# Performance work log

Measured on AMD Instinct MI355X. Metric: run time of the kernel, lower is better.

## Reference

```python
import jax, jax.numpy as jnp
import numpy as np

G = 4
N = G * G  # 16 nodes

def _edges():
    e = []
    for i in range(G):
        for j in range(G):
            n = i * G + j
            if j + 1 < G:
                e += [[n, n + 1], [n + 1, n]]
            if i + 1 < G:
                e += [[n, n + G], [n + G, n]]
    # PyG GATConv default add_self_loops=True
    e += [[k, k] for k in range(N)]
    a = np.asarray(e, dtype=np.int32)
    return jnp.asarray(a[:, 0]), jnp.asarray(a[:, 1])

SRC, DST = _edges()  # [E]=64 each


def gat_layer(h, W, att_src, att_dst, bias, concat):
    # h: [B, N, Fin]; W: [Fin, H*C]; att_*: [H, C]
    B = h.shape[0]
    H, C = att_src.shape
    x = (h @ W).reshape(B, N, H, C)
    a_s = (x * att_src).sum(-1)  # [B, N, H]
    a_d = (x * att_dst).sum(-1)
    alpha = jax.nn.leaky_relu(a_s[:, SRC] + a_d[:, DST], negative_slope=0.2)  # [B, E, H]
    alpha = jnp.swapaxes(alpha, 0, 1)  # [E, B, H] (segment ops act on axis 0)
    m = jax.ops.segment_max(alpha, DST, num_segments=N)  # [N, B, H]
    ex = jnp.exp(alpha - m[DST])
    s = jax.ops.segment_sum(ex, DST, num_segments=N)
    w = ex / s[DST]  # softmax over incoming edges per dst node
    msg = w[..., None] * jnp.swapaxes(x, 0, 1)[SRC]  # [E, B, H, C]
    agg = jax.ops.segment_sum(msg, DST, num_segments=N)  # [N, B, H, C]
    agg = jnp.swapaxes(agg, 0, 1)  # [B, N, H, C]
    if concat:
        return agg.reshape(B, N, H * C) + bias
    return agg.mean(axis=2) + bias


def layer_norm(x, g, b, eps=1e-5):
    mu = x.mean(-1, keepdims=True)
    var = ((x - mu) ** 2).mean(-1, keepdims=True)
    return (x - mu) * jax.lax.rsqrt(var + eps) * g + b


def setup_inputs() -> dict:
    key = jax.random.key(0)
    ks = iter(jax.random.split(key, 32))
    B, Cin, Hd, Hh, Dout = 8192, 16, 64, 4, 256
    def gl(k, shape, fan_in):
        return jax.random.normal(k, shape, jnp.float32) * (1.0 / np.sqrt(fan_in))
    inp = {
        'x': jax.random.normal(next(ks), (B, Cin, G, G), jnp.float32),
        'w_in': gl(next(ks), (Cin, Hd), Cin),
        'b_in': jnp.zeros((Hd,), jnp.float32),
        # GAT layer 0: 64 -> 4x64 concat
        'w0': gl(next(ks), (Hd, Hh * Hd), Hd),
        'as0': gl(next(ks), (Hh, Hd), Hd), 'ad0': gl(next(ks), (Hh, Hd), Hd),
        'bias0': jnp.zeros((Hh * Hd,), jnp.float32),
        # GAT layer 1: 256 -> 4x64 concat
        'w1': gl(next(ks), (Hh * Hd, Hh * Hd), Hh * Hd),
        'as1': gl(next(ks), (Hh, Hd), Hd), 'ad1': gl(next(ks), (Hh, Hd), Hd),
        'bias1': jnp.zeros((Hh * Hd,), jnp.float32),
        # GAT layer 2: 256 -> 64 (mean over heads)
        'w2': gl(next(ks), (Hh * Hd, Hh * Hd), Hh * Hd),
        'as2': gl(next(ks), (Hh, Hd), Hd), 'ad2': gl(next(ks), (Hh, Hd), Hd),
        'bias2': jnp.zeros((Hd,), jnp.float32),
        # output MLP: 64 -> 128 -> 256, LN+ReLU after each layer
        'mw1': gl(next(ks), (Hd, Dout // 2), Hd), 'mb1': jnp.zeros((Dout // 2,), jnp.float32),
        'g1': jnp.ones((Dout // 2,), jnp.float32), 'be1': jnp.zeros((Dout // 2,), jnp.float32),
        'mw2': gl(next(ks), (Dout // 2, Dout), Dout // 2), 'mb2': jnp.zeros((Dout,), jnp.float32),
        'g2': jnp.ones((Dout,), jnp.float32), 'be2': jnp.zeros((Dout,), jnp.float32),
    }
    return inp


def reference(x, w_in, b_in, w0, as0, ad0, bias0, w1, as1, ad1, bias1,
              w2, as2, ad2, bias2, mw1, mb1, g1, be1, mw2, mb2, g2, be2):
    B = x.shape[0]
    # grid -> node features: (B,C,H,W) -> (B,H,W,C) -> (B,N,C)
    h = jnp.transpose(x, (0, 2, 3, 1)).reshape(B, N, -1)
    h = jax.nn.relu(h @ w_in + b_in)
    h = gat_layer(h, w0, as0, ad0, bias0, concat=True)
    h = jax.nn.relu(h)  # dropout inactive in eval
    h = gat_layer(h, w1, as1, ad1, bias1, concat=True)
    h = jax.nn.relu(h)
    h = gat_layer(h, w2, as2, ad2, bias2, concat=False)  # [B, N, 64]
    gr = h.mean(axis=1)  # global mean pool over the 16 nodes
    y = jax.nn.relu(layer_norm(gr @ mw1 + mb1, g1, be1))
    y = jax.nn.relu(layer_norm(y @ mw2 + mb2, g2, be2))
    return y
```

## Files before the change

### kernel.cpp

```cpp
#include <hip/hip_runtime.h>

typedef unsigned short u16;
typedef unsigned int   u32;
typedef __attribute__((ext_vector_type(8))) short bf16x8;
typedef __attribute__((ext_vector_type(4))) float f32x4;

#define GPB 4

__constant__ int ADJ_DEG[16] = {3,4,4,3, 4,5,5,4, 4,5,5,4, 3,4,4,3};
__constant__ int ADJ_SRC[16][5] = {
  {0,1,4,0,0},   {1,0,2,5,0},   {2,1,3,6,0},   {3,2,7,0,0},
  {4,5,0,8,0},   {5,4,6,1,9},   {6,5,7,2,10},  {7,6,3,11,0},
  {8,9,4,12,0},  {9,8,10,5,13}, {10,9,11,6,14},{11,10,7,15,0},
  {12,13,8,0,0}, {13,12,14,9,0},{14,13,15,10,0},{15,14,11,0,0}
};

struct SMem {
  char hA[64*512];
  char hBT[4*256*32];
  union {
    struct { float h0f[64][17]; float w_in_s[16][64]; } pre;
    struct { float asd[64][4][2]; char ptb[8192]; } post;
    struct { float grs[4][64]; float z1[4][128]; float red[2][8][2]; } mlp;
  } u;
};

__device__ __forceinline__ int swz(int row, int b) { return (row << 9) + (b ^ ((row & 7) << 4)); }
__device__ __forceinline__ u32 f2bf1(float x) {
  u32 u = __float_as_uint(x);
  return (u + 0x7fffu + ((u >> 16) & 1u)) >> 16;
}
__device__ __forceinline__ u32 pk(float a, float b) { return f2bf1(a) | (f2bf1(b) << 16); }
__device__ __forceinline__ float bflo(u32 u) { return __uint_as_float(u << 16); }
__device__ __forceinline__ float bfhi(u32 u) { return __uint_as_float(u & 0xffff0000u); }

template<int KC>
__device__ __forceinline__ void gemm_att(SMem& sm, const u16* __restrict__ wfrag,
                                         const float* __restrict__ as_g,
                                         const float* __restrict__ ad_g, int t) {
  const int lane = t & 63;
  const int wc = (t >> 6) & 3;
  const int wrh = t >> 8;
  const int l15 = lane & 15, lg = lane >> 4;
  const uint4* wsrc = (const uint4*)wfrag;

  f32x4 acc[4][2];
#pragma unroll
  for (int ct = 0; ct < 4; ++ct) {
    acc[ct][0] = (f32x4){0.f, 0.f, 0.f, 0.f};
    acc[ct][1] = (f32x4){0.f, 0.f, 0.f, 0.f};
  }

#pragma unroll
  for (int kc = 0; kc < KC; ++kc) {
    uint4 wfr[4];
#pragma unroll
    for (int ct = 0; ct < 4; ++ct)
      wfr[ct] = wsrc[(size_t)(((kc*16 + wc*4 + ct) << 6) + lane)];
    bf16x8 xfr[2];
#pragma unroll
    for (int rt = 0; rt < 2; ++rt)
      xfr[rt] = *(const bf16x8*)(sm.hA + swz(wrh*32 + rt*16 + l15, kc*64 + 16*lg));
#pragma unroll
    for (int ct = 0; ct < 4; ++ct) {
      bf16x8 wv = *(const bf16x8*)&wfr[ct];
#pragma unroll
      for (int rt = 0; rt < 2; ++rt)
        acc[ct][rt] = __builtin_amdgcn_mfma_f32_16x16x32_bf16(wv, xfr[rt], acc[ct][rt], 0, 0, 0);
    }
  }

  float s1[2] = {0.f, 0.f}, s2[2] = {0.f, 0.f};
#pragma unroll
  for (int ct = 0; ct < 4; ++ct) {
    const float4 av = *(const float4*)(as_g + wc*64 + ct*16 + lg*4);
    const float4 dv = *(const float4*)(ad_g + wc*64 + ct*16 + lg*4);
#pragma unroll
    for (int rt = 0; rt < 2; ++rt) {
      const f32x4 a = acc[ct][rt];
      s1[rt] += a[0]*av.x + a[1]*av.y + a[2]*av.z + a[3]*av.w;
      s2[rt] += a[0]*dv.x + a[1]*dv.y + a[2]*dv.z + a[3]*dv.w;
    }
  }
#pragma unroll
  for (int rt = 0; rt < 2; ++rt) {
    s1[rt] += __shfl_xor(s1[rt], 16); s1[rt] += __shfl_xor(s1[rt], 32);
    s2[rt] += __shfl_xor(s2[rt], 16); s2[rt] += __shfl_xor(s2[rt], 32);
  }

#pragma unroll
  for (int ct = 0; ct < 4; ++ct) {
    const int c0 = wc*64 + ct*16 + lg*4;
#pragma unroll
    for (int rt = 0; rt < 2; ++rt) {
      const int r = wrh*32 + rt*16 + l15;
      char* dst = sm.hBT + ((r >> 4) << 13) + ((r & 15) << 1);
#pragma unroll
      for (int i = 0; i < 4; ++i)
        *(u16*)(dst + (c0 + i)*32) = (u16)f2bf1(acc[ct][rt][i]);
    }
  }

  if (lg < 2) {
    float2 v; v.x = s1[lg]; v.y = s2[lg];
    *(float2*)&sm.u.post.asd[wrh*32 + lg*16 + l15][wc][0] = v;
  }
}

__device__ __forceinline__ void softmax_pt(SMem& sm, int t) {
  if (t < 256) {
    const int g = t >> 6, d = (t >> 2) & 15, h = t & 3;
    const int deg = ADJ_DEG[d];
    const float advl = sm.u.post.asd[(g << 4) + d][h][1];
    float al[5]; int srcs[5];
    float m = -1e30f;
#pragma unroll
    for (int k = 0; k < 5; ++k) {
      srcs[k] = (k < deg) ? ADJ_SRC[d][k] : 99;
      float v = 0.f;
      if (k < deg) {
        v = sm.u.post.asd[(g << 4) + ADJ_SRC[d][k]][h][0] + advl;
        v = (v > 0.f) ? v : 0.2f * v;
        m = fmaxf(m, v);
      }
      al[k] = v;
    }
    float ssum = 0.f;
#pragma unroll
    for (int k = 0; k < 5; ++k)
      if (k < deg) { const float e = __expf(al[k] - m); al[k] = e; ssum += e; }
    const float inv = 1.f / ssum;
    float p[16];
#pragma unroll
    for (int s = 0; s < 16; ++s) {
      float v = 0.f;
#pragma unroll
      for (int k = 0; k < 5; ++k) v = (srcs[k] == s) ? al[k] * inv : v;
      p[s] = v;
    }
    uint4 lo, hi;
    lo.x = pk(p[0],p[1]);   lo.y = pk(p[2],p[3]);   lo.z = pk(p[4],p[5]);   lo.w = pk(p[6],p[7]);
    hi.x = pk(p[8],p[9]);   hi.y = pk(p[10],p[11]); hi.z = pk(p[12],p[13]); hi.w = pk(p[14],p[15]);
    char* pt = sm.u.post.ptb + (((g*4 + h)*32 + d) << 4);
    *(uint4*)pt = lo;
    *(uint4*)(pt + 256) = hi;
  }
}

template<int MODE>
__device__ __forceinline__ void aggregate_mfma(SMem& sm, const float* __restrict__ bias, int t) {
  const int lane = t & 63, w = t >> 6;
  const int g = w >> 1, l15 = lane & 15, lg = lane >> 4;
  const bf16x8 zero8 = {0,0,0,0,0,0,0,0};

  if (MODE == 0) {
#pragma unroll
    for (int hp = 0; hp < 2; ++hp) {
      const int h = (w & 1)*2 + hp;
      bf16x8 b = zero8;
      if (lane < 32) b = *(const bf16x8*)(sm.u.post.ptb + (((g*4 + h)*32 + lane) << 4));
#pragma unroll
      for (int ctile = 0; ctile < 4; ++ctile) {
        bf16x8 a = zero8;
        if (lane < 32) {
          const int c_row = h*64 + ctile*16 + l15;
          a = *(const bf16x8*)(sm.hBT + (g << 13) + c_row*32 + lg*16);
        }
        f32x4 acc = {0.f, 0.f, 0.f, 0.f};
        acc = __builtin_amdgcn_mfma_f32_16x16x32_bf16(a, b, acc, 0, 0, 0);
        const int c0 = h*64 + ctile*16 + lg*4;
        const float4 bv = *(const float4*)(bias + c0);
        uint2 o;
        o.x = pk(fmaxf(acc[0] + bv.x, 0.f), fmaxf(acc[1] + bv.y, 0.f));
        o.y = pk(fmaxf(acc[2] + bv.z, 0.f), fmaxf(acc[3] + bv.w, 0.f));
        *(uint2*)(sm.hA + swz(g*16 + l15, 2*c0)) = o;
      }
    }
  } else {
    const int half = w & 1;
    float (*o64)[68] = (float (*)[68])sm.hA;
#pragma unroll
    for (int ct2 = 0; ct2 < 2; ++ct2) {
      f32x4 acc = {0.f, 0.f, 0.f, 0.f};
#pragma unroll
      for (int h = 0; h < 4; ++h) {
        bf16x8 a = zero8, b = zero8;
        if (lane < 32) {
          b = *(const bf16x8*)(sm.u.post.ptb + (((g*4 + h)*32 + lane) << 4));
          const int c_row = h*64 + half*32 + ct2*16 + l15;
          a = *(const bf16x8*)(sm.hBT + (g << 13) + c_row*32 + lg*16);
        }
        acc = __builtin_amdgcn_mfma_f32_16x16x32_bf16(a, b, acc, 0, 0, 0);
      }
      const int ci = half*32 + ct2*16 + lg*4;
      const float4 bv = *(const float4*)(bias + ci);
      float4 ov;
      ov.x = fmaf(0.25f, acc[0], bv.x);
      ov.y = fmaf(0.25f, acc[1], bv.y);
      ov.z = fmaf(0.25f, acc[2], bv.z);
      ov.w = fmaf(0.25f, acc[3], bv.w);
      *(float4*)&o64[(g << 4) + l15][ci] = ov;
    }
  }
}

extern "C" __global__ void __launch_bounds__(512, 4)
gat_main(const float* __restrict__ xg,
         const float* __restrict__ w_in, const float* __restrict__ b_in,
         const float* __restrict__ as0, const float* __restrict__ ad0, const float* __restrict__ bias0,
         const float* __restrict__ as1, const float* __restrict__ ad1, const float* __restrict__ bias1,
         const float* __restrict__ as2, const float* __restrict__ ad2, const float* __restrict__ bias2,
         const u16* __restrict__ wf0, const u16* __restrict__ wf1, const u16* __restrict__ wf2,
         const float* __restrict__ mw1, const float* __restrict__ mb1,
         const float* __restrict__ g1, const float* __restrict__ be1,
         const u32* __restrict__ mwb2, const float* __restrict__ mb2,
         const float* __restrict__ g2, const float* __restrict__ be2,
         float* __restrict__ out, int Btot)
{
  __shared__ SMem sm;
  const int t = threadIdx.x;
  const int b0 = blockIdx.x * GPB;
  if (b0 >= Btot) return;

  if (t < 256) {
    const float4 v = *(const float4*)(xg + (size_t)b0*256 + 4*t);
    const int flat = 4*t, g = flat >> 8, rem = flat & 255;
    const int c = rem >> 4, n0 = rem & 15;
    sm.u.pre.h0f[(g << 4) + n0 + 0][c] = v.x;
    sm.u.pre.h0f[(g << 4) + n0 + 1][c] = v.y;
    sm.u.pre.h0f[(g << 4) + n0 + 2][c] = v.z;
    sm.u.pre.h0f[(g << 4) + n0 + 3][c] = v.w;
    ((float4*)sm.u.pre.w_in_s)[t] = ((const float4*)w_in)[t];
  }
  __syncthreads();

  {
    const int r = t >> 3, q = t & 7;
    const float4 bA = *(const float4*)(b_in + 8*q);
    const float4 bB = *(const float4*)(b_in + 8*q + 4);
    float a0=bA.x,a1=bA.y,a2=bA.z,a3=bA.w,a4=bB.x,a5=bB.y,a6=bB.z,a7=bB.w;
#pragma unroll
    for (int k = 0; k < 16; ++k) {
      const float hv = sm.u.pre.h0f[r][k];
      const float4 wA = *(const float4*)(&sm.u.pre.w_in_s[k][8*q]);
      const float4 wB = *(const float4*)(&sm.u.pre.w_in_s[k][8*q + 4]);
      a0 = fmaf(hv, wA.x, a0); a1 = fmaf(hv, wA.y, a1);
      a2 = fmaf(hv, wA.z, a2); a3 = fmaf(hv, wA.w, a3);
      a4 = fmaf(hv, wB.x, a4); a5 = fmaf(hv, wB.y, a5);
      a6 = fmaf(hv, wB.z, a6); a7 = fmaf(hv, wB.w, a7);
    }
    uint4 uo;
    uo.x = pk(fmaxf(a0,0.f), fmaxf(a1,0.f));
    uo.y = pk(fmaxf(a2,0.f), fmaxf(a3,0.f));
    uo.z = pk(fmaxf(a4,0.f), fmaxf(a5,0.f));
    uo.w = pk(fmaxf(a6,0.f), fmaxf(a7,0.f));
    *(uint4*)(sm.hA + swz(r, 16*q)) = uo;
  }
  __syncthreads();

  gemm_att<2>(sm, wf0, as0, ad0, t);  __syncthreads();
  softmax_pt(sm, t);                  __syncthreads();
  aggregate_mfma<0>(sm, bias0, t);    __syncthreads();

  gemm_att<8>(sm, wf1, as1, ad1, t);  __syncthreads();
  softmax_pt(sm, t);                  __syncthreads();
  aggregate_mfma<0>(sm, bias1, t);    __syncthreads();

  gemm_att<8>(sm, wf2, as2, ad2, t);  __syncthreads();
  softmax_pt(sm, t);                  __syncthreads();
  aggregate_mfma<1>(sm, bias2, t);    __syncthreads();

  if (t < 256) {
    const int g = t >> 6, col = t & 63;
    const float (*o64)[68] = (const float (*)[68])sm.hA;
    float s = 0.f;
#pragma unroll
    for (int r = 0; r < 16; ++r) s += o64[(g << 4) + r][col];
    sm.u.mlp.grs[g][col] = s * (1.f/16.f);
  }
  __syncthreads();

  const int mg = t >> 7, o = t & 127, w = t >> 6, lane = t & 63;
  float a = mb1[o];
#pragma unroll 8
  for (int k = 0; k < 64; ++k) a = fmaf(sm.u.mlp.grs[mg][k], mw1[k*128 + o], a);
  float su = a, sq = a*a;
#pragma unroll
  for (int off = 32; off >= 1; off >>= 1) { su += __shfl_xor(su, off); sq += __shfl_xor(sq, off); }
  if (lane == 0) { sm.u.mlp.red[0][w][0] = su; sm.u.mlp.red[0][w][1] = sq; }
  __syncthreads();
  {
    const float mu = (sm.u.mlp.red[0][2*mg][0] + sm.u.mlp.red[0][2*mg+1][0]) * (1.f/128.f);
    const float mq = (sm.u.mlp.red[0][2*mg][1] + sm.u.mlp.red[0][2*mg+1][1]) * (1.f/128.f);
    const float rstd = rsqrtf(mq - mu*mu + 1e-5f);
    sm.u.mlp.z1[mg][o] = fmaxf((a - mu)*rstd*g1[o] + be1[o], 0.f);
  }
  __syncthreads();
  {
    const float2 bb2 = *(const float2*)(mb2 + 2*o);
    float c0 = bb2.x, c1 = bb2.y;
#pragma unroll 8
    for (int k = 0; k < 128; ++k) {
      const float zk = sm.u.mlp.z1[mg][k];
      const u32 uw = mwb2[k*128 + o];
      c0 = fmaf(zk, bflo(uw), c0);
      c1 = fmaf(zk, bfhi(uw), c1);
    }
    float su2 = c0 + c1, sq2 = c0*c0 + c1*c1;
#pragma unroll
    for (int off = 32; off >= 1; off >>= 1) { su2 += __shfl_xor(su2, off); sq2 += __shfl_xor(sq2, off); }
    if (lane == 0) { sm.u.mlp.red[1][w][0] = su2; sm.u.mlp.red[1][w][1] = sq2; }
    __syncthreads();
    const float mu = (sm.u.mlp.red[1][2*mg][0] + sm.u.mlp.red[1][2*mg+1][0]) * (1.f/256.f);
    const float mq = (sm.u.mlp.red[1][2*mg][1] + sm.u.mlp.red[1][2*mg+1][1]) * (1.f/256.f);
    const float rstd = rsqrtf(mq - mu*mu + 1e-5f);
    const float2 gg2  = *(const float2*)(g2  + 2*o);
    const float2 bbe2 = *(const float2*)(be2 + 2*o);
    float2 ov;
    ov.x = fmaxf((c0 - mu)*rstd*gg2.x + bbe2.x, 0.f);
    ov.y = fmaxf((c1 - mu)*rstd*gg2.y + bbe2.y, 0.f);
    *(float2*)(out + (size_t)(b0 + mg)*256 + 2*o) = ov;
  }
}

__global__ void __launch_bounds__(256)
prep_w(const float* __restrict__ w0, const float* __restrict__ w1,
       const float* __restrict__ w2, const float* __restrict__ mw2,
       u16* __restrict__ wf) {
  const int f = blockIdx.x*256 + threadIdx.x;
  if (f >= 180224) return;
  if (f >= 147456) { wf[f] = (u16)f2bf1(mw2[f - 147456]); return; }
  const float* W; int local;
  if (f < 16384)      { W = w0; local = f; }
  else if (f < 81920) { W = w1; local = f - 16384; }
  else                { W = w2; local = f - 81920; }
  const int kc = local >> 13, nt = (local >> 9) & 15, lane = (local >> 3) & 63, j = local & 7;
  wf[f] = (u16)f2bf1(W[(kc*32 + (lane >> 4)*8 + j)*256 + nt*16 + (lane & 15)]);
}

extern "C" void kernel_launch(void* const* d_in, const int* in_sizes, int n_in,
                              void* d_out, int out_size, void* d_ws, size_t ws_size,
                              hipStream_t stream) {
  (void)n_in; (void)out_size; (void)ws_size;
  const float* xg   = (const float*)d_in[0];
  const float* w_in = (const float*)d_in[1];
  const float* b_in = (const float*)d_in[2];
  const float* w0   = (const float*)d_in[3];
  const float* as0  = (const float*)d_in[4];
  const float* ad0  = (const float*)d_in[5];
  const float* bi0  = (const float*)d_in[6];
  const float* w1   = (const float*)d_in[7];
  const float* as1  = (const float*)d_in[8];
  const float* ad1  = (const float*)d_in[9];
  const float* bi1  = (const float*)d_in[10];
  const float* w2   = (const float*)d_in[11];
  const float* as2  = (const float*)d_in[12];
  const float* ad2  = (const float*)d_in[13];
  const float* bi2  = (const float*)d_in[14];
  const float* mw1  = (const float*)d_in[15];
  const float* mb1  = (const float*)d_in[16];
  const float* g1   = (const float*)d_in[17];
  const float* be1  = (const float*)d_in[18];
  const float* mw2  = (const float*)d_in[19];
  const float* mb2  = (const float*)d_in[20];
  const float* g2   = (const float*)d_in[21];
  const float* be2  = (const float*)d_in[22];
  float* out = (float*)d_out;

  const int Btot = in_sizes[0] / 256;
  u16* wf = (u16*)d_ws;
  const u32* mwb2 = (const u32*)(wf + 147456);

  hipLaunchKernelGGL(prep_w, dim3(704), dim3(256), 0, stream, w0, w1, w2, mw2, wf);

  const int nblocks = (Btot + GPB - 1) / GPB;
  hipLaunchKernelGGL(gat_main, dim3(nblocks), dim3(512), 0, stream,
                     xg, w_in, b_in, as0, ad0, bi0, as1, ad1, bi1,
                     as2, ad2, bi2, wf, wf + 16384, wf + 81920,
                     mw1, mb1, g1, be1, mwb2, mb2, g2, be2, out, Btot);
}
```

Baseline: 174.1 us.

## Fold attention vectors into weights as extra MFMA tile, halve graphs per block

Precomputes W·att_src and W·att_dst per head in the weight prep kernel and appends them as a 17th column tile, so attention logits come out of one extra MFMA instead of a per-lane dot product plus shuffle reduction. Each block now handles 2 graphs instead of 4 with occupancy hint raised to 8 blocks per CU. The hBT layout gets a new XOR swizzle to cut LDS bank conflicts. bf16 packing switches to the HIP intrinsic. In exchange, attention logits are rounded to bf16, and half of the threads sit idle in the MLP tail.

```diff
diff --git a/kernel.cpp b/kernel.cpp
--- a/kernel.cpp
+++ b/kernel.cpp
@@ -1,11 +1,12 @@
 #include <hip/hip_runtime.h>
+#include <hip/hip_bf16.h>
 
 typedef unsigned short u16;
 typedef unsigned int   u32;
 typedef __attribute__((ext_vector_type(8))) short bf16x8;
 typedef __attribute__((ext_vector_type(4))) float f32x4;
 
-#define GPB 4
+#define GPB 2
 
 __constant__ int ADJ_DEG[16] = {3,4,4,3, 4,5,5,4, 4,5,5,4, 3,4,4,3};
 __constant__ int ADJ_SRC[16][5] = {
@@ -16,99 +17,73 @@
 };
 
 struct SMem {
-  char hA[64*512];
-  char hBT[4*256*32];
+  char hA[32*512];
+  char hBT[2*256*32];
   union {
-    struct { float h0f[64][17]; float w_in_s[16][64]; } pre;
-    struct { float asd[64][4][2]; char ptb[8192]; } post;
-    struct { float grs[4][64]; float z1[4][128]; float red[2][8][2]; } mlp;
+    struct { float h0f[32][17]; } pre;
+    struct { float asd[32][4][2]; char ptb[8*32*16]; } post;
+    struct { float grs[2][64]; float z1[2][128]; float red[2][8][2]; } mlp;
   } u;
 };
 
 __device__ __forceinline__ int swz(int row, int b) { return (row << 9) + (b ^ ((row & 7) << 4)); }
+__device__ __forceinline__ int xswz(int g, int c, int b) {
+  return (g << 13) + (c << 5) + (b ^ (((c >> 2) & 3) << 3));
+}
 __device__ __forceinline__ u32 f2bf1(float x) {
   u32 u = __float_as_uint(x);
   return (u + 0x7fffu + ((u >> 16) & 1u)) >> 16;
 }
-__device__ __forceinline__ u32 pk(float a, float b) { return f2bf1(a) | (f2bf1(b) << 16); }
-__device__ __forceinline__ float bflo(u32 u) { return __uint_as_float(u << 16); }
-__device__ __forceinline__ float bfhi(u32 u) { return __uint_as_float(u & 0xffff0000u); }
+__device__ __forceinline__ u32 pk2(float a, float b) {
+  __hip_bfloat162 h2 = __float22bfloat162_rn(make_float2(a, b));
+  union { __hip_bfloat162 h; u32 u; } cv; cv.h = h2; return cv.u;
+}
 
 template<int KC>
-__device__ __forceinline__ void gemm_att(SMem& sm, const u16* __restrict__ wfrag,
-                                         const float* __restrict__ as_g,
-                                         const float* __restrict__ ad_g, int t) {
-  const int lane = t & 63;
-  const int wc = (t >> 6) & 3;
-  const int wrh = t >> 8;
+__device__ __forceinline__ void gemm_att(SMem& sm, const uint4* __restrict__ wsrc, int t) {
+  const int lane = t & 63, w = t >> 6;
+  const int g = w >> 2, nt0 = (w & 3) * 4;
   const int l15 = lane & 15, lg = lane >> 4;
-  const uint4* wsrc = (const uint4*)wfrag;
-
-  f32x4 acc[4][2];
+  const bool hasAtt = (nt0 == 0);
+
+  f32x4 acc[4]; f32x4 accA = {0.f, 0.f, 0.f, 0.f};
+#pragma unroll
+  for (int ct = 0; ct < 4; ++ct) acc[ct] = (f32x4){0.f, 0.f, 0.f, 0.f};
+
+#pragma unroll
+  for (int kc = 0; kc < KC; ++kc) {
+    uint4 bw[4];
+#pragma unroll
+    for (int ct = 0; ct < 4; ++ct)
+      bw[ct] = wsrc[(kc*17 + nt0 + ct)*64 + lane];
+    uint4 ba;
+    if (hasAtt) ba = wsrc[(kc*17 + 16)*64 + lane];
+    const bf16x8 a = *(const bf16x8*)(sm.hA + swz(g*16 + l15, kc*64 + lg*16));
+#pragma unroll
+    for (int ct = 0; ct < 4; ++ct)
+      acc[ct] = __builtin_amdgcn_mfma_f32_16x16x32_bf16(a, *(const bf16x8*)&bw[ct], acc[ct], 0, 0, 0);
+    if (hasAtt)
+      accA = __builtin_amdgcn_mfma_f32_16x16x32_bf16(a, *(const bf16x8*)&ba, accA, 0, 0, 0);
+  }
+
 #pragma unroll
   for (int ct = 0; ct < 4; ++ct) {
-    acc[ct][0] = (f32x4){0.f, 0.f, 0.f, 0.f};
-    acc[ct][1] = (f32x4){0.f, 0.f, 0.f, 0.f};
-  }
-
-#pragma unroll
-  for (int kc = 0; kc < KC; ++kc) {
-    uint4 wfr[4];
-#pragma unroll
-    for (int ct = 0; ct < 4; ++ct)
-      wfr[ct] = wsrc[(size_t)(((kc*16 + wc*4 + ct) << 6) + lane)];
-    bf16x8 xfr[2];
-#pragma unroll
-    for (int rt = 0; rt < 2; ++rt)
-      xfr[rt] = *(const bf16x8*)(sm.hA + swz(wrh*32 + rt*16 + l15, kc*64 + 16*lg));
-#pragma unroll
-    for (int ct = 0; ct < 4; ++ct) {
-      bf16x8 wv = *(const bf16x8*)&wfr[ct];
-#pragma unroll
-      for (int rt = 0; rt < 2; ++rt)
-        acc[ct][rt] = __builtin_amdgcn_mfma_f32_16x16x32_bf16(wv, xfr[rt], acc[ct][rt], 0, 0, 0);
-    }
-  }
-
-  float s1[2] = {0.f, 0.f}, s2[2] = {0.f, 0.f};
-#pragma unroll
-  for (int ct = 0; ct < 4; ++ct) {
-    const float4 av = *(const float4*)(as_g + wc*64 + ct*16 + lg*4);
-    const float4 dv = *(const float4*)(ad_g + wc*64 + ct*16 + lg*4);
-#pragma unroll
-    for (int rt = 0; rt < 2; ++rt) {
-      const f32x4 a = acc[ct][rt];
-      s1[rt] += a[0]*av.x + a[1]*av.y + a[2]*av.z + a[3]*av.w;
-      s2[rt] += a[0]*dv.x + a[1]*dv.y + a[2]*dv.z + a[3]*dv.w;
-    }
-  }
-#pragma unroll
-  for (int rt = 0; rt < 2; ++rt) {
-    s1[rt] += __shfl_xor(s1[rt], 16); s1[rt] += __shfl_xor(s1[rt], 32);
-    s2[rt] += __shfl_xor(s2[rt], 16); s2[rt] += __shfl_xor(s2[rt], 32);
-  }
-
-#pragma unroll
-  for (int ct = 0; ct < 4; ++ct) {
-    const int c0 = wc*64 + ct*16 + lg*4;
-#pragma unroll
-    for (int rt = 0; rt < 2; ++rt) {
-      const int r = wrh*32 + rt*16 + l15;
-      char* dst = sm.hBT + ((r >> 4) << 13) + ((r & 15) << 1);
-#pragma unroll
-      for (int i = 0; i < 4; ++i)
-        *(u16*)(dst + (c0 + i)*32) = (u16)f2bf1(acc[ct][rt][i]);
-    }
-  }
-
-  if (lg < 2) {
-    float2 v; v.x = s1[lg]; v.y = s2[lg];
-    *(float2*)&sm.u.post.asd[wrh*32 + lg*16 + l15][wc][0] = v;
+    const int c = (nt0 + ct)*16 + l15;
+    uint2 o;
+    o.x = pk2(acc[ct][0], acc[ct][1]);
+    o.y = pk2(acc[ct][2], acc[ct][3]);
+    *(uint2*)(sm.hBT + xswz(g, c, lg*8)) = o;
+  }
+  if (hasAtt && l15 < 8) {
+    const int h = l15 & 3, sd = l15 >> 2;
+#pragma unroll
+    for (int reg = 0; reg < 4; ++reg)
+      sm.u.post.asd[g*16 + lg*4 + reg][h][sd] = accA[reg];
   }
 }
 
 __device__ __forceinline__ void softmax_pt(SMem& sm, int t) {
-  if (t < 256) {
+  if (t < 128) {
     const int g = t >> 6, d = (t >> 2) & 15, h = t & 3;
     const int deg = ADJ_DEG[d];
     const float advl = sm.u.post.asd[(g << 4) + d][h][1];
@@ -139,8 +114,8 @@
       p[s] = v;
     }
     uint4 lo, hi;
-    lo.x = pk(p[0],p[1]);   lo.y = pk(p[2],p[3]);   lo.z = pk(p[4],p[5]);   lo.w = pk(p[6],p[7]);
-    hi.x = pk(p[8],p[9]);   hi.y = pk(p[10],p[11]); hi.z = pk(p[12],p[13]); hi.w = pk(p[14],p[15]);
+    lo.x = pk2(p[0],p[1]);   lo.y = pk2(p[2],p[3]);   lo.z = pk2(p[4],p[5]);   lo.w = pk2(p[6],p[7]);
+    hi.x = pk2(p[8],p[9]);   hi.y = pk2(p[10],p[11]); hi.z = pk2(p[12],p[13]); hi.w = pk2(p[14],p[15]);
     char* pt = sm.u.post.ptb + (((g*4 + h)*32 + d) << 4);
     *(uint4*)pt = lo;
     *(uint4*)(pt + 256) = hi;
@@ -150,67 +125,67 @@
 template<int MODE>
 __device__ __forceinline__ void aggregate_mfma(SMem& sm, const float* __restrict__ bias, int t) {
   const int lane = t & 63, w = t >> 6;
-  const int g = w >> 1, l15 = lane & 15, lg = lane >> 4;
+  const int g = w >> 2, l15 = lane & 15, lg = lane >> 4;
   const bf16x8 zero8 = {0,0,0,0,0,0,0,0};
 
   if (MODE == 0) {
-#pragma unroll
-    for (int hp = 0; hp < 2; ++hp) {
-      const int h = (w & 1)*2 + hp;
-      bf16x8 b = zero8;
-      if (lane < 32) b = *(const bf16x8*)(sm.u.post.ptb + (((g*4 + h)*32 + lane) << 4));
-#pragma unroll
-      for (int ctile = 0; ctile < 4; ++ctile) {
-        bf16x8 a = zero8;
-        if (lane < 32) {
-          const int c_row = h*64 + ctile*16 + l15;
-          a = *(const bf16x8*)(sm.hBT + (g << 13) + c_row*32 + lg*16);
-        }
-        f32x4 acc = {0.f, 0.f, 0.f, 0.f};
-        acc = __builtin_amdgcn_mfma_f32_16x16x32_bf16(a, b, acc, 0, 0, 0);
-        const int c0 = h*64 + ctile*16 + lg*4;
-        const float4 bv = *(const float4*)(bias + c0);
-        uint2 o;
-        o.x = pk(fmaxf(acc[0] + bv.x, 0.f), fmaxf(acc[1] + bv.y, 0.f));
-        o.y = pk(fmaxf(acc[2] + bv.z, 0.f), fmaxf(acc[3] + bv.w, 0.f));
-        *(uint2*)(sm.hA + swz(g*16 + l15, 2*c0)) = o;
+    const int h = w & 3;
+    bf16x8 b = zero8;
+    if (lane < 32) b = *(const bf16x8*)(sm.u.post.ptb + (((g*4 + h)*32 + lane) << 4));
+#pragma unroll
+    for (int ct = 0; ct < 4; ++ct) {
+      bf16x8 a = zero8;
+      if (lane < 32) {
+        const int c = h*64 + ct*16 + l15;
+        union { uint2 u2[2]; bf16x8 v; } cv;
+        cv.u2[0] = *(const uint2*)(sm.hBT + xswz(g, c, lg*16));
+        cv.u2[1] = *(const uint2*)(sm.hBT + xswz(g, c, lg*16 + 8));
+        a = cv.v;
       }
+      f32x4 acc = {0.f, 0.f, 0.f, 0.f};
+      acc = __builtin_amdgcn_mfma_f32_16x16x32_bf16(a, b, acc, 0, 0, 0);
+      const int c0 = h*64 + ct*16 + lg*4;
+      const float4 bv = *(const float4*)(bias + c0);
+      uint2 o;
+      o.x = pk2(fmaxf(acc[0] + bv.x, 0.f), fmaxf(acc[1] + bv.y, 0.f));
+      o.y = pk2(fmaxf(acc[2] + bv.z, 0.f), fmaxf(acc[3] + bv.w, 0.f));
+      *(uint2*)(sm.hA + swz(g*16 + l15, 2*c0)) = o;
     }
   } else {
-    const int half = w & 1;
+    const int ct = w & 3;
+    f32x4 acc = {0.f, 0.f, 0.f, 0.f};
+#pragma unroll
+    for (int h = 0; h < 4; ++h) {
+      bf16x8 a = zero8, b = zero8;
+      if (lane < 32) {
+        b = *(const bf16x8*)(sm.u.post.ptb + (((g*4 + h)*32 + lane) << 4));
+        const int c = h*64 + ct*16 + l15;
+        union { uint2 u2[2]; bf16x8 v; } cv;
+        cv.u2[0] = *(const uint2*)(sm.hBT + xswz(g, c, lg*16));
+        cv.u2[1] = *(const uint2*)(sm.hBT + xswz(g, c, lg*16 + 8));
+        a = cv.v;
+      }
+      acc = __builtin_amdgcn_mfma_f32_16x16x32_bf16(a, b, acc, 0, 0, 0);
+    }
     float (*o64)[68] = (float (*)[68])sm.hA;
-#pragma unroll
-    for (int ct2 = 0; ct2 < 2; ++ct2) {
-      f32x4 acc = {0.f, 0.f, 0.f, 0.f};
-#pragma unroll
-      for (int h = 0; h < 4; ++h) {
-        bf16x8 a = zero8, b = zero8;
-        if (lane < 32) {
-          b = *(const bf16x8*)(sm.u.post.ptb + (((g*4 + h)*32 + lane) << 4));
-          const int c_row = h*64 + half*32 + ct2*16 + l15;
-          a = *(const bf16x8*)(sm.hBT + (g << 13) + c_row*32 + lg*16);
-        }
-        acc = __builtin_amdgcn_mfma_f32_16x16x32_bf16(a, b, acc, 0, 0, 0);
-      }
-      const int ci = half*32 + ct2*16 + lg*4;
-      const float4 bv = *(const float4*)(bias + ci);
-      float4 ov;
-      ov.x = fmaf(0.25f, acc[0], bv.x);
-      ov.y = fmaf(0.25f, acc[1], bv.y);
-      ov.z = fmaf(0.25f, acc[2], bv.z);
-      ov.w = fmaf(0.25f, acc[3], bv.w);
-      *(float4*)&o64[(g << 4) + l15][ci] = ov;
-    }
-  }
-}
-
-extern "C" __global__ void __launch_bounds__(512, 4)
+    const int ci = ct*16 + lg*4;
+    const float4 bv = *(const float4*)(bias + ci);
+    float4 ov;
+    ov.x = fmaf(0.25f, acc[0], bv.x);
+    ov.y = fmaf(0.25f, acc[1], bv.y);
+    ov.z = fmaf(0.25f, acc[2], bv.z);
+    ov.w = fmaf(0.25f, acc[3], bv.w);
+    *(float4*)&o64[(g << 4) + l15][ci] = ov;
+  }
+}
+
+extern "C" __global__ void __launch_bounds__(512, 8)
 gat_main(const float* __restrict__ xg,
          const float* __restrict__ w_in, const float* __restrict__ b_in,
-         const float* __restrict__ as0, const float* __restrict__ ad0, const float* __restrict__ bias0,
-         const float* __restrict__ as1, const float* __restrict__ ad1, const float* __restrict__ bias1,
-         const float* __restrict__ as2, const float* __restrict__ ad2, const float* __restrict__ bias2,
-         const u16* __restrict__ wf0, const u16* __restrict__ wf1, const u16* __restrict__ wf2,
+         const float* __restrict__ bias0, const float* __restrict__ bias1,
+         const float* __restrict__ bias2,
+         const uint4* __restrict__ wq0, const uint4* __restrict__ wq1,
+         const uint4* __restrict__ wq2,
          const float* __restrict__ mw1, const float* __restrict__ mb1,
          const float* __restrict__ g1, const float* __restrict__ be1,
          const u32* __restrict__ mwb2, const float* __restrict__ mb2,
@@ -222,55 +197,46 @@
   const int b0 = blockIdx.x * GPB;
   if (b0 >= Btot) return;
 
-  if (t < 256) {
-    const float4 v = *(const float4*)(xg + (size_t)b0*256 + 4*t);
-    const int flat = 4*t, g = flat >> 8, rem = flat & 255;
-    const int c = rem >> 4, n0 = rem & 15;
-    sm.u.pre.h0f[(g << 4) + n0 + 0][c] = v.x;
-    sm.u.pre.h0f[(g << 4) + n0 + 1][c] = v.y;
-    sm.u.pre.h0f[(g << 4) + n0 + 2][c] = v.z;
-    sm.u.pre.h0f[(g << 4) + n0 + 3][c] = v.w;
-    ((float4*)sm.u.pre.w_in_s)[t] = ((const float4*)w_in)[t];
-  }
-  __syncthreads();
-
   {
-    const int r = t >> 3, q = t & 7;
-    const float4 bA = *(const float4*)(b_in + 8*q);
-    const float4 bB = *(const float4*)(b_in + 8*q + 4);
-    float a0=bA.x,a1=bA.y,a2=bA.z,a3=bA.w,a4=bB.x,a5=bB.y,a6=bB.z,a7=bB.w;
+    const float v = xg[(size_t)b0*256 + t];
+    const int g = t >> 8, c = (t >> 4) & 15, n = t & 15;
+    sm.u.pre.h0f[(g << 4) + n][c] = v;
+  }
+  if (t < 256) ((float4*)sm.hBT)[t] = ((const float4*)w_in)[t];
+  __syncthreads();
+
+  {
+    const int r = t >> 4, q = t & 15;
+    const float* w_s = (const float*)sm.hBT;
+    const float4 bi = *(const float4*)(b_in + 4*q);
+    float a0 = bi.x, a1 = bi.y, a2 = bi.z, a3 = bi.w;
 #pragma unroll
     for (int k = 0; k < 16; ++k) {
       const float hv = sm.u.pre.h0f[r][k];
-      const float4 wA = *(const float4*)(&sm.u.pre.w_in_s[k][8*q]);
-      const float4 wB = *(const float4*)(&sm.u.pre.w_in_s[k][8*q + 4]);
-      a0 = fmaf(hv, wA.x, a0); a1 = fmaf(hv, wA.y, a1);
-      a2 = fmaf(hv, wA.z, a2); a3 = fmaf(hv, wA.w, a3);
-      a4 = fmaf(hv, wB.x, a4); a5 = fmaf(hv, wB.y, a5);
-      a6 = fmaf(hv, wB.z, a6); a7 = fmaf(hv, wB.w, a7);
-    }
-    uint4 uo;
-    uo.x = pk(fmaxf(a0,0.f), fmaxf(a1,0.f));
-    uo.y = pk(fmaxf(a2,0.f), fmaxf(a3,0.f));
-    uo.z = pk(fmaxf(a4,0.f), fmaxf(a5,0.f));
-    uo.w = pk(fmaxf(a6,0.f), fmaxf(a7,0.f));
-    *(uint4*)(sm.hA + swz(r, 16*q)) = uo;
-  }
-  __syncthreads();
-
-  gemm_att<2>(sm, wf0, as0, ad0, t);  __syncthreads();
-  softmax_pt(sm, t);                  __syncthreads();
-  aggregate_mfma<0>(sm, bias0, t);    __syncthreads();
-
-  gemm_att<8>(sm, wf1, as1, ad1, t);  __syncthreads();
-  softmax_pt(sm, t);                  __syncthreads();
-  aggregate_mfma<0>(sm, bias1, t);    __syncthreads();
-
-  gemm_att<8>(sm, wf2, as2, ad2, t);  __syncthreads();
-  softmax_pt(sm, t);                  __syncthreads();
-  aggregate_mfma<1>(sm, bias2, t);    __syncthreads();
-
-  if (t < 256) {
+      const float4 wv = *(const float4*)(w_s + k*64 + 4*q);
+      a0 = fmaf(hv, wv.x, a0); a1 = fmaf(hv, wv.y, a1);
+      a2 = fmaf(hv, wv.z, a2); a3 = fmaf(hv, wv.w, a3);
+    }
+    uint2 o;
+    o.x = pk2(fmaxf(a0, 0.f), fmaxf(a1, 0.f));
+    o.y = pk2(fmaxf(a2, 0.f), fmaxf(a3, 0.f));
+    *(uint2*)(sm.hA + swz(r, 8*q)) = o;
+  }
+  __syncthreads();
+
+  gemm_att<2>(sm, wq0, t);        __syncthreads();
+  softmax_pt(sm, t);              __syncthreads();
+  aggregate_mfma<0>(sm, bias0, t); __syncthreads();
+
+  gemm_att<8>(sm, wq1, t);        __syncthreads();
+  softmax_pt(sm, t);              __syncthreads();
+  aggregate_mfma<0>(sm, bias1, t); __syncthreads();
+
+  gemm_att<8>(sm, wq2, t);        __syncthreads();
+  softmax_pt(sm, t);              __syncthreads();
+  aggregate_mfma<1>(sm, bias2, t); __syncthreads();
+
+  if (t < 128) {
     const int g = t >> 6, col = t & 63;
     const float (*o64)[68] = (const float (*)[68])sm.hA;
     float s = 0.f;
@@ -280,62 +246,91 @@
   }
   __syncthreads();
 
-  const int mg = t >> 7, o = t & 127, w = t >> 6, lane = t & 63;
-  float a = mb1[o];
+  float a1v = 0.f;
+  if (t < 256) {
+    const int mg = t >> 7, o = t & 127;
+    a1v = mb1[o];
 #pragma unroll 8
-  for (int k = 0; k < 64; ++k) a = fmaf(sm.u.mlp.grs[mg][k], mw1[k*128 + o], a);
-  float su = a, sq = a*a;
-#pragma unroll
-  for (int off = 32; off >= 1; off >>= 1) { su += __shfl_xor(su, off); sq += __shfl_xor(sq, off); }
-  if (lane == 0) { sm.u.mlp.red[0][w][0] = su; sm.u.mlp.red[0][w][1] = sq; }
-  __syncthreads();
-  {
+    for (int k = 0; k < 64; ++k) a1v = fmaf(sm.u.mlp.grs[mg][k], mw1[k*128 + o], a1v);
+    float su = a1v, sq = a1v*a1v;
+#pragma unroll
+    for (int off = 32; off >= 1; off >>= 1) { su += __shfl_xor(su, off); sq += __shfl_xor(sq, off); }
+    if ((t & 63) == 0) { sm.u.mlp.red[0][t >> 6][0] = su; sm.u.mlp.red[0][t >> 6][1] = sq; }
+  }
+  __syncthreads();
+  if (t < 256) {
+    const int mg = t >> 7, o = t & 127;
     const float mu = (sm.u.mlp.red[0][2*mg][0] + sm.u.mlp.red[0][2*mg+1][0]) * (1.f/128.f);
     const float mq = (sm.u.mlp.red[0][2*mg][1] + sm.u.mlp.red[0][2*mg+1][1]) * (1.f/128.f);
     const float rstd = rsqrtf(mq - mu*mu + 1e-5f);
-    sm.u.mlp.z1[mg][o] = fmaxf((a - mu)*rstd*g1[o] + be1[o], 0.f);
-  }
-  __syncthreads();
-  {
-    const float2 bb2 = *(const float2*)(mb2 + 2*o);
-    float c0 = bb2.x, c1 = bb2.y;
+    sm.u.mlp.z1[mg][o] = fmaxf((a1v - mu)*rstd*g1[o] + be1[o], 0.f);
+  }
+  __syncthreads();
+
+  float c0 = 0.f, c1 = 0.f;
+  if (t < 256) {
+    const int mg = t >> 7, op = t & 127;
+    const float2 bb2 = *(const float2*)(mb2 + 2*op);
+    c0 = bb2.x; c1 = bb2.y;
 #pragma unroll 8
     for (int k = 0; k < 128; ++k) {
       const float zk = sm.u.mlp.z1[mg][k];
-      const u32 uw = mwb2[k*128 + o];
-      c0 = fmaf(zk, bflo(uw), c0);
-      c1 = fmaf(zk, bfhi(uw), c1);
-    }
-    float su2 = c0 + c1, sq2 = c0*c0 + c1*c1;
-#pragma unroll
-    for (int off = 32; off >= 1; off >>= 1) { su2 += __shfl_xor(su2, off); sq2 += __shfl_xor(sq2, off); }
-    if (lane == 0) { sm.u.mlp.red[1][w][0] = su2; sm.u.mlp.red[1][w][1] = sq2; }
-    __syncthreads();
+      const u32 uw = mwb2[k*128 + op];
+      c0 = fmaf(zk, __uint_as_float(uw << 16), c0);
+      c1 = fmaf(zk, __uint_as_float(uw & 0xffff0000u), c1);
+    }
+    float su = c0 + c1, sq = c0*c0 + c1*c1;
+#pragma unroll
+    for (int off = 32; off >= 1; off >>= 1) { su += __shfl_xor(su, off); sq += __shfl_xor(sq, off); }
+    if ((t & 63) == 0) { sm.u.mlp.red[1][t >> 6][0] = su; sm.u.mlp.red[1][t >> 6][1] = sq; }
+  }
+  __syncthreads();
+  if (t < 256) {
+    const int mg = t >> 7, op = t & 127;
     const float mu = (sm.u.mlp.red[1][2*mg][0] + sm.u.mlp.red[1][2*mg+1][0]) * (1.f/256.f);
     const float mq = (sm.u.mlp.red[1][2*mg][1] + sm.u.mlp.red[1][2*mg+1][1]) * (1.f/256.f);
     const float rstd = rsqrtf(mq - mu*mu + 1e-5f);
-    const float2 gg2  = *(const float2*)(g2  + 2*o);
-    const float2 bbe2 = *(const float2*)(be2 + 2*o);
+    const float2 gg2  = *(const float2*)(g2  + 2*op);
+    const float2 bbe2 = *(const float2*)(be2 + 2*op);
     float2 ov;
     ov.x = fmaxf((c0 - mu)*rstd*gg2.x + bbe2.x, 0.f);
     ov.y = fmaxf((c1 - mu)*rstd*gg2.y + bbe2.y, 0.f);
-    *(float2*)(out + (size_t)(b0 + mg)*256 + 2*o) = ov;
+    *(float2*)(out + (size_t)(b0 + mg)*256 + 2*op) = ov;
   }
 }
 
 __global__ void __launch_bounds__(256)
-prep_w(const float* __restrict__ w0, const float* __restrict__ w1,
-       const float* __restrict__ w2, const float* __restrict__ mw2,
-       u16* __restrict__ wf) {
+prep_w(const float* __restrict__ w0, const float* __restrict__ as0, const float* __restrict__ ad0,
+       const float* __restrict__ w1, const float* __restrict__ as1, const float* __restrict__ ad1,
+       const float* __restrict__ w2, const float* __restrict__ as2, const float* __restrict__ ad2,
+       const float* __restrict__ mw2, u16* __restrict__ wf) {
   const int f = blockIdx.x*256 + threadIdx.x;
-  if (f >= 180224) return;
-  if (f >= 147456) { wf[f] = (u16)f2bf1(mw2[f - 147456]); return; }
-  const float* W; int local;
-  if (f < 16384)      { W = w0; local = f; }
-  else if (f < 81920) { W = w1; local = f - 16384; }
-  else                { W = w2; local = f - 81920; }
-  const int kc = local >> 13, nt = (local >> 9) & 15, lane = (local >> 3) & 63, j = local & 7;
-  wf[f] = (u16)f2bf1(W[(kc*32 + (lane >> 4)*8 + j)*256 + nt*16 + (lane & 15)]);
+  if (f >= 189440) return;
+  if (f >= 156672) { wf[f] = (u16)f2bf1(mw2[f - 156672]); return; }
+  const float *W, *as_, *ad_; int local;
+  if (f < 17408)      { W = w0; as_ = as0; ad_ = ad0; local = f; }
+  else if (f < 87040) { W = w1; as_ = as1; ad_ = ad1; local = f - 17408; }
+  else                { W = w2; as_ = as2; ad_ = ad2; local = f - 87040; }
+  const int kc = local / 8704;
+  const int r  = local - kc*8704;
+  const int nt = r >> 9;
+  const int lane = (r >> 3) & 63;
+  const int j = r & 7;
+  const int k = kc*32 + (lane >> 4)*8 + j;
+  const int l15 = lane & 15;
+  float val;
+  if (nt < 16) {
+    val = W[k*256 + nt*16 + l15];
+  } else if (l15 < 8) {
+    const int h = l15 & 3;
+    const float* av = (l15 < 4) ? as_ : ad_;
+    float s = 0.f;
+    for (int c = 0; c < 64; ++c) s = fmaf(W[k*256 + h*64 + c], av[h*64 + c], s);
+    val = s;
+  } else {
+    val = 0.f;
+  }
+  wf[f] = (u16)f2bf1(val);
 }
 
 extern "C" void kernel_launch(void* const* d_in, const int* in_sizes, int n_in,
@@ -369,13 +364,16 @@
 
   const int Btot = in_sizes[0] / 256;
   u16* wf = (u16*)d_ws;
-  const u32* mwb2 = (const u32*)(wf + 147456);
-
-  hipLaunchKernelGGL(prep_w, dim3(704), dim3(256), 0, stream, w0, w1, w2, mw2, wf);
+  const uint4* wq0 = (const uint4*)wf;
+  const uint4* wq1 = (const uint4*)(wf + 17408);
+  const uint4* wq2 = (const uint4*)(wf + 87040);
+  const u32* mwb2  = (const u32*)(wf + 156672);
+
+  hipLaunchKernelGGL(prep_w, dim3(740), dim3(256), 0, stream,
+                     w0, as0, ad0, w1, as1, ad1, w2, as2, ad2, mw2, wf);
 
   const int nblocks = (Btot + GPB - 1) / GPB;
   hipLaunchKernelGGL(gat_main, dim3(nblocks), dim3(512), 0, stream,
-                     xg, w_in, b_in, as0, ad0, bi0, as1, ad1, bi1,
-                     as2, ad2, bi2, wf, wf + 16384, wf + 81920,
+                     xg, w_in, b_in, bi0, bi1, bi2, wq0, wq1, wq2,
                      mw1, mb1, g1, be1, mwb2, mb2, g2, be2, out, Btot);
 }
```

Measured after the change: 269.5 us. 54.8% more time.
